# Kernel tuning notes

Measured on AMD Instinct MI355X. Metric: run time of the kernel, lower is better.

The kernel has to match this reference:

```python
import jax, jax.numpy as jnp
import numpy as np

SCALE = 64.0
MARGIN = 0.35
LAMBDA = 0.4
GAMMA = 2
EPS = 1e-12


def _l2_normalize(v, axis=-1):
    n = jnp.sqrt(jnp.sum(v * v, axis=axis, keepdims=True))
    return v / jnp.maximum(n, EPS)


def setup_inputs() -> dict:
    key = jax.random.key(0)
    k1, k2, k3, k4 = jax.random.split(key, 4)
    B, D, C = 1024, 512, 100000
    stdv = 1.0 / np.sqrt(D)
    x = jax.random.normal(k1, (B, D), dtype=jnp.float32)
    target = jax.random.randint(k2, (B,), 0, C, dtype=jnp.int64)
    id_agent = jax.random.uniform(k3, (C, D), dtype=jnp.float32, minval=-stdv, maxval=stdv)
    b = jax.random.uniform(k4, (C, D), dtype=jnp.float32, minval=-stdv, maxval=stdv)
    return {"x": x, "target": target, "id_agent": id_agent, "b": b}


def reference(x, target, id_agent, b):
    B = x.shape[0]
    x_n = _l2_normalize(x, axis=1)              # [B, D]
    w = _l2_normalize(id_agent, axis=1)         # [C, D] (in-place normalize in torch)

    # discriminative loss
    w_batch = w[target]                          # [B, D] gather
    d = x_n - w_batch                            # displacement vectors
    bt = b[target]                               # [B, D]
    bt_norm = jnp.sqrt(jnp.sum(bt * bt, axis=1, keepdims=True))
    bt_norm_c = jnp.clip(bt_norm, 0.0, 0.05)
    bt_unit = bt / jnp.maximum(bt_norm, EPS)
    resid = d - bt_unit * bt_norm_c
    loss_disc = jnp.mean(jnp.sqrt(jnp.sum(resid * resid, axis=1)))

    # AM-softmax logits with margin on target class (training mode)
    score = x_n @ w.T                            # [B, C] large GEMM
    rows = jnp.arange(B)
    score = score.at[rows, target].add(-MARGIN)
    score = score * SCALE

    # focal cross-entropy: CE mean first, then focal modulation (as in source)
    logsm = jax.nn.log_softmax(score, axis=1)
    nll = -logsm[rows, target]
    logp = jnp.mean(nll)
    p = jnp.exp(-logp)
    loss_score = (1.0 - p) ** GAMMA * logp

    return (LAMBDA * loss_disc + loss_score)[None]  # shape [1]
```

## Files before the change

### kernel.cpp

```cpp
#include <hip/hip_runtime.h>
#include <hip/hip_bf16.h>

typedef __attribute__((ext_vector_type(4))) int i32x4;

#define B_N 1024
#define D_K 512
#define C_N 100000
#define SCALE_F 64.0f
#define MARGIN_F 0.35f
#define BM 128
#define BN 256
#define BKB 128
#define NT_ 391
#define MT_ 8
#define MAXL 64.0f
#define KQ (SCALE_F / (127.0f * 127.0f))

__device__ __forceinline__ float dot4(float4 a, float4 b) {
    return a.x * b.x + a.y * b.y + a.z * b.z + a.w * b.w;
}
__device__ __forceinline__ float amax4(float4 a) {
    return fmaxf(fmaxf(fabsf(a.x), fabsf(a.y)), fmaxf(fabsf(a.z), fabsf(a.w)));
}
__device__ __forceinline__ int packq(float v0, float v1, float v2, float v3, float qs) {
    int q0 = __float2int_rn(v0 * qs), q1 = __float2int_rn(v1 * qs);
    int q2 = __float2int_rn(v2 * qs), q3 = __float2int_rn(v3 * qs);
    return (q0 & 0xFF) | ((q1 & 0xFF) << 8) | ((q2 & 0xFF) << 16) | ((q3 & 0xFF) << 24);
}

__global__ void normx_disc_kernel(const float* __restrict__ x,
                                  const int* __restrict__ target,
                                  const float* __restrict__ ida,
                                  const float* __restrict__ bmat,
                                  char* __restrict__ xq,
                                  float* __restrict__ sx,
                                  float* __restrict__ dpart,
                                  float* __restrict__ tlogit,
                                  float* __restrict__ rowsum) {
    int row = blockIdx.x * 4 + (threadIdx.x >> 6);
    int l = threadIdx.x & 63;
    long t = (long)target[row];
    const float4* xp = (const float4*)(x + (size_t)row * D_K);
    const float4* wp = (const float4*)(ida + (size_t)t * D_K);
    const float4* bp = (const float4*)(bmat + (size_t)t * D_K);
    float4 x0 = xp[l], x1 = xp[64 + l];
    float4 w0 = wp[l], w1 = wp[64 + l];
    float4 b0 = bp[l], b1 = bp[64 + l];
    float xssq = dot4(x0, x0) + dot4(x1, x1);
    float wssq = dot4(w0, w0) + dot4(w1, w1);
    float bssq = dot4(b0, b0) + dot4(b1, b1);
    float xmx = fmaxf(amax4(x0), amax4(x1));
#pragma unroll
    for (int m = 1; m < 64; m <<= 1) {
        xssq += __shfl_xor(xssq, m);
        wssq += __shfl_xor(wssq, m);
        bssq += __shfl_xor(bssq, m);
        xmx = fmaxf(xmx, __shfl_xor(xmx, m));
    }
    float xinv = 1.0f / fmaxf(sqrtf(xssq), 1e-12f);
    float winv = 1.0f / fmaxf(sqrtf(wssq), 1e-12f);
    float btn = sqrtf(bssq);
    float cs = fminf(btn, 0.05f) / fmaxf(btn, 1e-12f);

    float sxm = fmaxf(xmx * xinv, 1e-12f);
    float qs = 127.0f / sxm * xinv;
    int* oq = (int*)(xq + (size_t)row * D_K);
    oq[l] = packq(x0.x, x0.y, x0.z, x0.w, qs);
    oq[64 + l] = packq(x1.x, x1.y, x1.z, x1.w, qs);

    float xs[8] = {x0.x, x0.y, x0.z, x0.w, x1.x, x1.y, x1.z, x1.w};
    float wv[8] = {w0.x, w0.y, w0.z, w0.w, w1.x, w1.y, w1.z, w1.w};
    float bv[8] = {b0.x, b0.y, b0.z, b0.w, b1.x, b1.y, b1.z, b1.w};
    float rss = 0.0f, dt = 0.0f;
#pragma unroll
    for (int i = 0; i < 8; ++i) {
        float xn = xs[i] * xinv;
        float wn = wv[i] * winv;
        float d = xn - wn;
        float r = d - bv[i] * cs;
        rss += r * r;
        dt += xn * wn;
    }
#pragma unroll
    for (int m = 1; m < 64; m <<= 1) {
        rss += __shfl_xor(rss, m);
        dt += __shfl_xor(dt, m);
    }
    if (l == 0) {
        sx[row] = sxm;
        dpart[row] = sqrtf(rss);
        tlogit[row] = SCALE_F * dt;
        rowsum[row] = 0.0f;
    }
}

__global__ void norm_w_kernel(const float* __restrict__ w,
                              char* __restrict__ wq,
                              float* __restrict__ sw) {
    int row = blockIdx.x * 4 + (threadIdx.x >> 6);
    int l = threadIdx.x & 63;
    const float4* rp = (const float4*)(w + (size_t)row * D_K);
    float4 a = rp[l], b = rp[64 + l];
    float ssq = dot4(a, a) + dot4(b, b);
    float mx = fmaxf(amax4(a), amax4(b));
#pragma unroll
    for (int m = 1; m < 64; m <<= 1) {
        ssq += __shfl_xor(ssq, m);
        mx = fmaxf(mx, __shfl_xor(mx, m));
    }
    float inv = 1.0f / fmaxf(sqrtf(ssq), 1e-12f);
    float swm = fmaxf(mx * inv, 1e-12f);
    float qs = 127.0f / swm * inv;
    int* oq = (int*)(wq + (size_t)row * D_K);
    oq[l] = packq(a.x, a.y, a.z, a.w, qs);
    oq[64 + l] = packq(b.x, b.y, b.z, b.w, qs);
    if (l == 0) sw[row] = swm;
}

__global__ __launch_bounds__(256, 2) void gemm_lse_kernel(const char* __restrict__ A,
                                                          const char* __restrict__ W,
                                                          const float* __restrict__ sx,
                                                          const float* __restrict__ sw,
                                                          float* __restrict__ rowsum) {
    __shared__ char As[BM * BKB];
    __shared__ char Bs[BN * BKB];
    __shared__ float sxl[BM];
    __shared__ float swl[BN];
    __shared__ float rs[2][BM];

    int tid = threadIdx.x;
    int wave = tid >> 6, l = tid & 63;
    int wm = wave >> 1, wn = wave & 1;

    int wgid = (blockIdx.x & 7) * NT_ + (blockIdx.x >> 3);
    int nt = wgid >> 3, mt = wgid & 7;
    int m0 = mt * BM, n0 = nt * BN;

    int srow = l >> 3;
    int scolB = ((l & 7) ^ (l >> 3)) * 16;

    {
        int c = n0 + tid;
        swl[tid] = sw[c < C_N ? c : C_N - 1];
        if (tid < BM) sxl[tid] = sx[m0 + tid];
    }

    i32x4 acc[4][8];
#pragma unroll
    for (int i = 0; i < 4; ++i)
#pragma unroll
        for (int j = 0; j < 8; ++j) acc[i][j] = (i32x4){0, 0, 0, 0};

    int cl = l & 15, hi = l >> 4;

    for (int kt = 0; kt < 4; ++kt) {
#pragma unroll
        for (int i = 0; i < 4; ++i) {
            int rb = wave * 32 + i * 8;
            const char* ga = A + (size_t)(m0 + rb + srow) * D_K + kt * BKB + scolB;
            __builtin_amdgcn_global_load_lds(
                (const __attribute__((address_space(1))) void*)ga,
                (__attribute__((address_space(3))) void*)&As[rb * BKB], 16, 0, 0);
        }
#pragma unroll
        for (int i = 0; i < 8; ++i) {
            int rb = wave * 64 + i * 8;
            int rn = n0 + rb + srow;
            rn = rn < C_N ? rn : C_N - 1;
            const char* gb = W + (size_t)rn * D_K + kt * BKB + scolB;
            __builtin_amdgcn_global_load_lds(
                (const __attribute__((address_space(1))) void*)gb,
                (__attribute__((address_space(3))) void*)&Bs[rb * BKB], 16, 0, 0);
        }
        __syncthreads();

#pragma unroll
        for (int kk = 0; kk < 2; ++kk) {
            int px = (((kk << 2) | hi) ^ (cl & 7)) * 16;
            i32x4 af[4], bfr[8];
#pragma unroll
            for (int mi = 0; mi < 4; ++mi)
                af[mi] = *(const i32x4*)&As[(wm * 64 + mi * 16 + cl) * BKB + px];
#pragma unroll
            for (int ni = 0; ni < 8; ++ni)
                bfr[ni] = *(const i32x4*)&Bs[(wn * 128 + ni * 16 + cl) * BKB + px];
#pragma unroll
            for (int mi = 0; mi < 4; ++mi)
#pragma unroll
                for (int ni = 0; ni < 8; ++ni)
                    acc[mi][ni] = __builtin_amdgcn_mfma_i32_16x16x64_i8(af[mi], bfr[ni], acc[mi][ni], 0, 0, 0);
        }
        __syncthreads();
    }

    float fcv[8];
    bool cok[8];
#pragma unroll
    for (int ni = 0; ni < 8; ++ni) {
        fcv[ni] = swl[wn * 128 + ni * 16 + cl];
        cok[ni] = (n0 + wn * 128 + ni * 16 + cl) < C_N;
    }

#pragma unroll
    for (int mi = 0; mi < 4; ++mi) {
#pragma unroll
        for (int j = 0; j < 4; ++j) {
            float fr = sxl[wm * 64 + mi * 16 + hi * 4 + j] * KQ;
            float se = 0.0f;
#pragma unroll
            for (int ni = 0; ni < 8; ++ni)
                if (cok[ni]) se += __expf((float)acc[mi][ni][j] * fr * fcv[ni] - MAXL);
#pragma unroll
            for (int xm = 1; xm < 16; xm <<= 1) se += __shfl_xor(se, xm);
            if (cl == 0) rs[wn][wm * 64 + mi * 16 + hi * 4 + j] = se;
        }
    }
    __syncthreads();
    if (tid < BM) {
        float s = rs[0][tid] + rs[1][tid];
        atomicAdd(&rowsum[m0 + tid], s);
    }
}

__global__ void rowfin_final_kernel(const float* __restrict__ rowsum,
                                    const float* __restrict__ tlogit,
                                    const float* __restrict__ dpart,
                                    float* __restrict__ out) {
    __shared__ float redn[16];
    __shared__ float redd[16];
    int tid = threadIdx.x;
    float lse = MAXL + logf(rowsum[tid]);
    float st = tlogit[tid];
    float corr = __expf(st - lse) * (__expf(-SCALE_F * MARGIN_F) - 1.0f);
    float lse2 = lse + log1pf(corr);
    float nll = lse2 - (st - SCALE_F * MARGIN_F);
    float dv = dpart[tid];
#pragma unroll
    for (int xm = 1; xm < 64; xm <<= 1) {
        nll += __shfl_xor(nll, xm);
        dv += __shfl_xor(dv, xm);
    }
    if ((tid & 63) == 0) {
        redn[tid >> 6] = nll;
        redd[tid >> 6] = dv;
    }
    __syncthreads();
    if (tid == 0) {
        float sn = 0.0f, sd = 0.0f;
#pragma unroll
        for (int i = 0; i < 16; ++i) { sn += redn[i]; sd += redd[i]; }
        float logp = sn * (1.0f / B_N);
        float disc = sd * (1.0f / B_N);
        float p = __expf(-logp);
        float om = 1.0f - p;
        out[0] = 0.4f * disc + om * om * logp;
    }
}

extern "C" void kernel_launch(void* const* d_in, const int* in_sizes, int n_in,
                              void* d_out, int out_size, void* d_ws, size_t ws_size,
                              hipStream_t stream) {
    const float* x = (const float*)d_in[0];
    const int* target = (const int*)d_in[1];
    const float* ida = (const float*)d_in[2];
    const float* bmat = (const float*)d_in[3];
    float* out = (float*)d_out;

    char* ws = (char*)d_ws;
    size_t off = 0;
    float* rowsum = (float*)(ws + off);  off += (size_t)B_N * 4;
    char* xq = (char*)(ws + off);        off += (size_t)B_N * D_K;
    char* wq = (char*)(ws + off);        off += (size_t)C_N * D_K;
    float* sx = (float*)(ws + off);      off += (size_t)B_N * 4;
    float* sw = (float*)(ws + off);      off += (size_t)C_N * 4;
    float* tlogit = (float*)(ws + off);  off += (size_t)B_N * 4;
    float* dpart = (float*)(ws + off);   off += (size_t)B_N * 4;

    normx_disc_kernel<<<B_N / 4, 256, 0, stream>>>(x, target, ida, bmat, xq, sx, dpart, tlogit, rowsum);
    norm_w_kernel<<<C_N / 4, 256, 0, stream>>>(ida, wq, sw);
    gemm_lse_kernel<<<MT_ * NT_, 256, 0, stream>>>(xq, wq, sx, sw, rowsum);
    rowfin_final_kernel<<<1, 1024, 0, stream>>>(rowsum, tlogit, dpart, out);
}
```

Baseline: 139.5 us.

## Fuse W normalization into persistent GEMM kernel with per-tile readiness flags

```diff
diff --git a/kernel.cpp b/kernel.cpp
--- a/kernel.cpp
+++ b/kernel.cpp
@@ -11,10 +11,12 @@
 #define BM 128
 #define BN 256
 #define BKB 128
-#define NT_ 391
-#define MT_ 8
+#define NGRP 391
+#define GRID 512
 #define MAXL 64.0f
-#define KQ (SCALE_F / (127.0f * 127.0f))
+#define LOG2E 1.4426950408889634f
+#define KQ2 (SCALE_F / (127.0f * 127.0f) * LOG2E)
+#define MAXL2 (MAXL * LOG2E)
 
 __device__ __forceinline__ float dot4(float4 a, float4 b) {
     return a.x * b.x + a.y * b.y + a.z * b.z + a.w * b.w;
@@ -36,7 +38,11 @@
                                   float* __restrict__ sx,
                                   float* __restrict__ dpart,
                                   float* __restrict__ tlogit,
-                                  float* __restrict__ rowsum) {
+                                  float* __restrict__ rowsum,
+                                  int* __restrict__ flags) {
+    int gid = blockIdx.x * 256 + threadIdx.x;
+    if (gid < NGRP) flags[gid] = 0;
+
     int row = blockIdx.x * 4 + (threadIdx.x >> 6);
     int l = threadIdx.x & 63;
     long t = (long)target[row];
@@ -94,34 +100,13 @@
     }
 }
 
-__global__ void norm_w_kernel(const float* __restrict__ w,
-                              char* __restrict__ wq,
-                              float* __restrict__ sw) {
-    int row = blockIdx.x * 4 + (threadIdx.x >> 6);
-    int l = threadIdx.x & 63;
-    const float4* rp = (const float4*)(w + (size_t)row * D_K);
-    float4 a = rp[l], b = rp[64 + l];
-    float ssq = dot4(a, a) + dot4(b, b);
-    float mx = fmaxf(amax4(a), amax4(b));
-#pragma unroll
-    for (int m = 1; m < 64; m <<= 1) {
-        ssq += __shfl_xor(ssq, m);
-        mx = fmaxf(mx, __shfl_xor(mx, m));
-    }
-    float inv = 1.0f / fmaxf(sqrtf(ssq), 1e-12f);
-    float swm = fmaxf(mx * inv, 1e-12f);
-    float qs = 127.0f / swm * inv;
-    int* oq = (int*)(wq + (size_t)row * D_K);
-    oq[l] = packq(a.x, a.y, a.z, a.w, qs);
-    oq[64 + l] = packq(b.x, b.y, b.z, b.w, qs);
-    if (l == 0) sw[row] = swm;
-}
-
-__global__ __launch_bounds__(256, 2) void gemm_lse_kernel(const char* __restrict__ A,
-                                                          const char* __restrict__ W,
-                                                          const float* __restrict__ sx,
-                                                          const float* __restrict__ sw,
-                                                          float* __restrict__ rowsum) {
+__global__ __launch_bounds__(256, 2) void fused_gemm_kernel(const char* __restrict__ A,
+                                                            const float* __restrict__ Wf,
+                                                            const float* __restrict__ sx,
+                                                            char* __restrict__ wq,
+                                                            float* __restrict__ sw,
+                                                            int* __restrict__ flags,
+                                                            float* __restrict__ rowsum) {
     __shared__ char As[BM * BKB];
     __shared__ char Bs[BN * BKB];
     __shared__ float sxl[BM];
@@ -131,94 +116,133 @@
     int tid = threadIdx.x;
     int wave = tid >> 6, l = tid & 63;
     int wm = wave >> 1, wn = wave & 1;
-
-    int wgid = (blockIdx.x & 7) * NT_ + (blockIdx.x >> 3);
-    int nt = wgid >> 3, mt = wgid & 7;
-    int m0 = mt * BM, n0 = nt * BN;
-
+    int cl = l & 15, hi = l >> 4;
+    int b = blockIdx.x;
+
+    if (b < NGRP) {
+#pragma unroll 1
+        for (int it = 0; it < 64; ++it) {
+            int row = b * 256 + it * 4 + wave;
+            if (row < C_N) {
+                const float4* rp = (const float4*)(Wf + (size_t)row * D_K);
+                float4 a = rp[l], bb = rp[64 + l];
+                float ssq = dot4(a, a) + dot4(bb, bb);
+                float mx = fmaxf(amax4(a), amax4(bb));
+#pragma unroll
+                for (int m = 1; m < 64; m <<= 1) {
+                    ssq += __shfl_xor(ssq, m);
+                    mx = fmaxf(mx, __shfl_xor(mx, m));
+                }
+                float inv = 1.0f / fmaxf(sqrtf(ssq), 1e-12f);
+                float swm = fmaxf(mx * inv, 1e-12f);
+                float qs = 127.0f / swm * inv;
+                int* oq = (int*)(wq + (size_t)row * D_K);
+                oq[l] = packq(a.x, a.y, a.z, a.w, qs);
+                oq[64 + l] = packq(bb.x, bb.y, bb.z, bb.w, qs);
+                if (l == 0) sw[row] = swm;
+            }
+        }
+        __syncthreads();
+        if (tid == 0)
+            __hip_atomic_store(&flags[b], 1, __ATOMIC_RELEASE, __HIP_MEMORY_SCOPE_AGENT);
+    }
+
+    int c = b & 7, j = b >> 3;
     int srow = l >> 3;
     int scolB = ((l & 7) ^ (l >> 3)) * 16;
 
-    {
-        int c = n0 + tid;
-        swl[tid] = sw[c < C_N ? c : C_N - 1];
-        if (tid < BM) sxl[tid] = sx[m0 + tid];
-    }
-
-    i32x4 acc[4][8];
-#pragma unroll
-    for (int i = 0; i < 4; ++i)
-#pragma unroll
-        for (int j = 0; j < 8; ++j) acc[i][j] = (i32x4){0, 0, 0, 0};
-
-    int cl = l & 15, hi = l >> 4;
-
-    for (int kt = 0; kt < 4; ++kt) {
-#pragma unroll
-        for (int i = 0; i < 4; ++i) {
-            int rb = wave * 32 + i * 8;
-            const char* ga = A + (size_t)(m0 + rb + srow) * D_K + kt * BKB + scolB;
-            __builtin_amdgcn_global_load_lds(
-                (const __attribute__((address_space(1))) void*)ga,
-                (__attribute__((address_space(3))) void*)&As[rb * BKB], 16, 0, 0);
-        }
-#pragma unroll
-        for (int i = 0; i < 8; ++i) {
-            int rb = wave * 64 + i * 8;
-            int rn = n0 + rb + srow;
-            rn = rn < C_N ? rn : C_N - 1;
-            const char* gb = W + (size_t)rn * D_K + kt * BKB + scolB;
-            __builtin_amdgcn_global_load_lds(
-                (const __attribute__((address_space(1))) void*)gb,
-                (__attribute__((address_space(3))) void*)&Bs[rb * BKB], 16, 0, 0);
+#pragma unroll 1
+    for (int i = j; i < NGRP; i += 64) {
+        int wgid = c * NGRP + i;
+        int nt = wgid >> 3, mt = wgid & 7;
+        int m0 = mt * BM, n0 = nt * BN;
+
+        if (tid == 0) {
+            while (__hip_atomic_load(&flags[nt], __ATOMIC_ACQUIRE, __HIP_MEMORY_SCOPE_AGENT) == 0)
+                __builtin_amdgcn_s_sleep(2);
         }
         __syncthreads();
 
-#pragma unroll
-        for (int kk = 0; kk < 2; ++kk) {
-            int px = (((kk << 2) | hi) ^ (cl & 7)) * 16;
-            i32x4 af[4], bfr[8];
-#pragma unroll
-            for (int mi = 0; mi < 4; ++mi)
-                af[mi] = *(const i32x4*)&As[(wm * 64 + mi * 16 + cl) * BKB + px];
-#pragma unroll
-            for (int ni = 0; ni < 8; ++ni)
-                bfr[ni] = *(const i32x4*)&Bs[(wn * 128 + ni * 16 + cl) * BKB + px];
-#pragma unroll
-            for (int mi = 0; mi < 4; ++mi)
+        {
+            int cc = n0 + tid;
+            swl[tid] = sw[cc < C_N ? cc : C_N - 1];
+            if (tid < BM) sxl[tid] = sx[m0 + tid];
+        }
+
+        i32x4 acc[4][8];
+#pragma unroll
+        for (int mi = 0; mi < 4; ++mi)
+#pragma unroll
+            for (int ni = 0; ni < 8; ++ni) acc[mi][ni] = (i32x4){0, 0, 0, 0};
+
+#pragma unroll 1
+        for (int kt = 0; kt < 4; ++kt) {
+#pragma unroll
+            for (int u = 0; u < 4; ++u) {
+                int rb = wave * 32 + u * 8;
+                const char* ga = A + (size_t)(m0 + rb + srow) * D_K + kt * BKB + scolB;
+                __builtin_amdgcn_global_load_lds(
+                    (const __attribute__((address_space(1))) void*)ga,
+                    (__attribute__((address_space(3))) void*)&As[rb * BKB], 16, 0, 0);
+            }
+#pragma unroll
+            for (int u = 0; u < 8; ++u) {
+                int rb = wave * 64 + u * 8;
+                int rn = n0 + rb + srow;
+                rn = rn < C_N ? rn : C_N - 1;
+                const char* gb = wq + (size_t)rn * D_K + kt * BKB + scolB;
+                __builtin_amdgcn_global_load_lds(
+                    (const __attribute__((address_space(1))) void*)gb,
+                    (__attribute__((address_space(3))) void*)&Bs[rb * BKB], 16, 0, 0);
+            }
+            __syncthreads();
+
+#pragma unroll
+            for (int kk = 0; kk < 2; ++kk) {
+                int px = (((kk << 2) | hi) ^ (cl & 7)) * 16;
+                i32x4 af[4], bfr[8];
+#pragma unroll
+                for (int mi = 0; mi < 4; ++mi)
+                    af[mi] = *(const i32x4*)&As[(wm * 64 + mi * 16 + cl) * BKB + px];
 #pragma unroll
                 for (int ni = 0; ni < 8; ++ni)
-                    acc[mi][ni] = __builtin_amdgcn_mfma_i32_16x16x64_i8(af[mi], bfr[ni], acc[mi][ni], 0, 0, 0);
+                    bfr[ni] = *(const i32x4*)&Bs[(wn * 128 + ni * 16 + cl) * BKB + px];
+#pragma unroll
+                for (int mi = 0; mi < 4; ++mi)
+#pragma unroll
+                    for (int ni = 0; ni < 8; ++ni)
+                        acc[mi][ni] = __builtin_amdgcn_mfma_i32_16x16x64_i8(af[mi], bfr[ni], acc[mi][ni], 0, 0, 0);
+            }
+            __syncthreads();
+        }
+
+        float fcv[8];
+        bool cok[8];
+#pragma unroll
+        for (int ni = 0; ni < 8; ++ni) {
+            fcv[ni] = swl[wn * 128 + ni * 16 + cl];
+            cok[ni] = (n0 + wn * 128 + ni * 16 + cl) < C_N;
+        }
+#pragma unroll
+        for (int mi = 0; mi < 4; ++mi) {
+#pragma unroll
+            for (int jj = 0; jj < 4; ++jj) {
+                float fr = sxl[wm * 64 + mi * 16 + hi * 4 + jj] * KQ2;
+                float se = 0.0f;
+#pragma unroll
+                for (int ni = 0; ni < 8; ++ni)
+                    if (cok[ni]) se += exp2f((float)acc[mi][ni][jj] * fr * fcv[ni] - MAXL2);
+#pragma unroll
+                for (int xm = 1; xm < 16; xm <<= 1) se += __shfl_xor(se, xm);
+                if (cl == 0) rs[wn][wm * 64 + mi * 16 + hi * 4 + jj] = se;
+            }
         }
         __syncthreads();
-    }
-
-    float fcv[8];
-    bool cok[8];
-#pragma unroll
-    for (int ni = 0; ni < 8; ++ni) {
-        fcv[ni] = swl[wn * 128 + ni * 16 + cl];
-        cok[ni] = (n0 + wn * 128 + ni * 16 + cl) < C_N;
-    }
-
-#pragma unroll
-    for (int mi = 0; mi < 4; ++mi) {
-#pragma unroll
-        for (int j = 0; j < 4; ++j) {
-            float fr = sxl[wm * 64 + mi * 16 + hi * 4 + j] * KQ;
-            float se = 0.0f;
-#pragma unroll
-            for (int ni = 0; ni < 8; ++ni)
-                if (cok[ni]) se += __expf((float)acc[mi][ni][j] * fr * fcv[ni] - MAXL);
-#pragma unroll
-            for (int xm = 1; xm < 16; xm <<= 1) se += __shfl_xor(se, xm);
-            if (cl == 0) rs[wn][wm * 64 + mi * 16 + hi * 4 + j] = se;
-        }
-    }
-    __syncthreads();
-    if (tid < BM) {
-        float s = rs[0][tid] + rs[1][tid];
-        atomicAdd(&rowsum[m0 + tid], s);
+        if (tid < BM) {
+            float s = rs[0][tid] + rs[1][tid];
+            atomicAdd(&rowsum[m0 + tid], s);
+        }
+        __syncthreads();
     }
 }
 
@@ -275,9 +299,10 @@
     float* sw = (float*)(ws + off);      off += (size_t)C_N * 4;
     float* tlogit = (float*)(ws + off);  off += (size_t)B_N * 4;
     float* dpart = (float*)(ws + off);   off += (size_t)B_N * 4;
-
-    normx_disc_kernel<<<B_N / 4, 256, 0, stream>>>(x, target, ida, bmat, xq, sx, dpart, tlogit, rowsum);
-    norm_w_kernel<<<C_N / 4, 256, 0, stream>>>(ida, wq, sw);
-    gemm_lse_kernel<<<MT_ * NT_, 256, 0, stream>>>(xq, wq, sx, sw, rowsum);
+    int* flags = (int*)(ws + off);       off += (size_t)NGRP * 4;
+
+    normx_disc_kernel<<<B_N / 4, 256, 0, stream>>>(x, target, ida, bmat, xq, sx, dpart,
+                                                   tlogit, rowsum, flags);
+    fused_gemm_kernel<<<GRID, 256, 0, stream>>>(xq, ida, sx, wq, sw, flags, rowsum);
     rowfin_final_kernel<<<1, 1024, 0, stream>>>(rowsum, tlogit, dpart, out);
 }
```

After: 245.0 us. +75.7%, slower.
